# Performance work log

Measured on AMD Instinct MI355X. Metric: run time of the kernel, lower is better.

Reference implementation:

```python
import jax, jax.numpy as jnp
import numpy as np

N_NODES = 100000
N_EDGES = 3200000
N_GRAPHS = 64
HEADS = 8
NEG_SLOPE = 0.2


def gat_conv(x, W, a_src, a_dst, b, src, dst, heads, out_ch):
    """PyG GATConv (concat=True, add_self_loops=True, negative_slope=0.2, eval mode).
    x: [N, F_in]; W: [F_in, heads*out_ch]; a_src/a_dst: [heads, out_ch]; b: [heads*out_ch].
    src/dst already include self loops. Softmax over edges sharing a dst node.
    """
    n = x.shape[0]
    h = (x @ W).reshape(n, heads, out_ch)            # [N, H, C]
    alpha_src = jnp.einsum('nhc,hc->nh', h, a_src)   # [N, H]
    alpha_dst = jnp.einsum('nhc,hc->nh', h, a_dst)   # [N, H]
    e = jax.nn.leaky_relu(alpha_src[src] + alpha_dst[dst], NEG_SLOPE)  # [E, H]
    m = jax.ops.segment_max(e, dst, num_segments=n)
    e = jnp.exp(e - m[dst])
    denom = jax.ops.segment_sum(e, dst, num_segments=n)
    alpha = e / (denom[dst] + 1e-16)                 # [E, H]
    msg = alpha[:, :, None] * h[src]                 # [E, H, C]
    out = jax.ops.segment_sum(msg, dst, num_segments=n)  # [N, H, C]
    return out.reshape(n, heads * out_ch) + b


def setup_inputs() -> dict:
    key = jax.random.key(0)
    ks = jax.random.split(key, 24)
    x = jax.random.normal(ks[0], (N_NODES, 128), dtype=jnp.float32)
    edge_index = jax.random.randint(ks[1], (2, N_EDGES), 0, N_NODES, dtype=jnp.int32)
    batch = jnp.sort(jax.random.randint(ks[2], (N_NODES,), 0, N_GRAPHS, dtype=jnp.int32))

    def glorot(k, shape):
        fan_in, fan_out = shape[0], shape[-1]
        lim = np.sqrt(6.0 / (fan_in + fan_out)).astype(np.float32)
        return jax.random.uniform(k, shape, jnp.float32, -lim, lim)

    params = {
        'W1': glorot(ks[3], (128, 64)),
        'a_src1': glorot(ks[4], (HEADS, 8)),
        'a_dst1': glorot(ks[5], (HEADS, 8)),
        'b1': jnp.zeros((64,), jnp.float32),
        'W2': glorot(ks[6], (64, 128)),
        'a_src2': glorot(ks[7], (HEADS, 16)),
        'a_dst2': glorot(ks[8], (HEADS, 16)),
        'b2': jnp.zeros((128,), jnp.float32),
        'fc1_w': glorot(ks[9], (128, 256)),  'fc1_b': jnp.zeros((256,), jnp.float32),
        'fc2_w': glorot(ks[10], (256, 512)), 'fc2_b': jnp.zeros((512,), jnp.float32),
        'fc3_w': glorot(ks[11], (512, 512)), 'fc3_b': jnp.zeros((512,), jnp.float32),
        'fc4_w': glorot(ks[12], (512, 100)), 'fc4_b': jnp.zeros((100,), jnp.float32),
    }
    return {'x': x, 'edge_index': edge_index, 'batch': batch, **params}


def reference(x, edge_index, batch,
              W1, a_src1, a_dst1, b1,
              W2, a_src2, a_dst2, b2,
              fc1_w, fc1_b, fc2_w, fc2_b, fc3_w, fc3_b, fc4_w, fc4_b):
    n = x.shape[0]
    loop = jnp.arange(n, dtype=edge_index.dtype)
    src = jnp.concatenate([edge_index[0], loop])
    dst = jnp.concatenate([edge_index[1], loop])

    h = gat_conv(x, W1, a_src1, a_dst1, b1, src, dst, HEADS, 8)
    h = jax.nn.relu(h)
    h = gat_conv(h, W2, a_src2, a_dst2, b2, src, dst, HEADS, 16)
    h = jax.nn.relu(h)

    # global_mean_pool over batch ids
    sums = jax.ops.segment_sum(h, batch, num_segments=N_GRAPHS)        # [G, 128]
    counts = jax.ops.segment_sum(jnp.ones((n,), h.dtype), batch, num_segments=N_GRAPHS)
    g = sums / jnp.maximum(counts, 1.0)[:, None]

    g = jax.nn.relu(g @ fc1_w + fc1_b)
    g = jax.nn.relu(g @ fc2_w + fc2_b)
    g = jax.nn.relu(g @ fc3_w + fc3_b)
    g = g @ fc4_w + fc4_b
    return g.reshape(-1, 10, 10)
```

## Files before the change

### kernel.cpp

```cpp
#include <hip/hip_runtime.h>
#include <hip/hip_bf16.h>

#define NN 100000
#define NE 3200000
#define ET (NE + NN)
#define NG 64
#define BINBITS 10
#define NBINS 98
#define EPB 16
#define LOG2E 1.44269504088896f

__device__ __forceinline__ unsigned bfr(float x) {
  unsigned u = __float_as_uint(x);
  return (u + 0x7FFFu + ((u >> 16) & 1u)) >> 16;
}

__device__ __forceinline__ unsigned fkey(float x) {
  unsigned b = __float_as_uint(x);
  return (b & 0x80000000u) ? ~b : (b | 0x80000000u);
}

__device__ __forceinline__ float gmax_decode(unsigned k) {
  return __uint_as_float((k & 0x80000000u) ? (k & 0x7FFFFFFFu) : ~k);
}

__global__ void init_counts_k(int* counts) {
  int i = blockIdx.x * 256 + threadIdx.x;
  if (i < NN) counts[i] = 1;
}

__global__ void count_k(const int* __restrict__ dst, int* __restrict__ counts) {
  int i = blockIdx.x * 256 + threadIdx.x;
  if (i < NE) atomicAdd(&counts[dst[i]], 1);
}

__global__ __launch_bounds__(1024) void scan1_k(const int* __restrict__ cnt, int* __restrict__ csum) {
  __shared__ int lds[1024];
  int i = blockIdx.x * 1024 + threadIdx.x;
  lds[threadIdx.x] = (i < NN) ? cnt[i] : 0;
  __syncthreads();
  for (int off = 512; off > 0; off >>= 1) {
    if (threadIdx.x < off) lds[threadIdx.x] += lds[threadIdx.x + off];
    __syncthreads();
  }
  if (threadIdx.x == 0) csum[blockIdx.x] = lds[0];
}

__global__ __launch_bounds__(128) void scan2_k(int* csum, int nch) {
  __shared__ int lds[128];
  int v = (threadIdx.x < nch) ? csum[threadIdx.x] : 0;
  lds[threadIdx.x] = v;
  __syncthreads();
  for (int off = 1; off < 128; off <<= 1) {
    int t = (threadIdx.x >= off) ? lds[threadIdx.x - off] : 0;
    __syncthreads();
    lds[threadIdx.x] += t;
    __syncthreads();
  }
  if (threadIdx.x < nch) csum[threadIdx.x] = lds[threadIdx.x] - v;
}

__global__ __launch_bounds__(1024) void scan3_k(const int* __restrict__ cnt, const int* __restrict__ csum,
                                                int* __restrict__ indptr, int* __restrict__ cursor) {
  __shared__ int lds[1024];
  int i = blockIdx.x * 1024 + threadIdx.x;
  int v = (i < NN) ? cnt[i] : 0;
  lds[threadIdx.x] = v;
  __syncthreads();
  for (int off = 1; off < 1024; off <<= 1) {
    int t = (threadIdx.x >= off) ? lds[threadIdx.x - off] : 0;
    __syncthreads();
    lds[threadIdx.x] += t;
    __syncthreads();
  }
  int excl = csum[blockIdx.x] + lds[threadIdx.x] - v;
  if (i < NN) { indptr[i] = excl; cursor[i] = excl; }
  else if (i == NN) indptr[NN] = ET;
}

__global__ void bininit_k(const int* __restrict__ indptr, int* __restrict__ binbase, int* __restrict__ bincur) {
  int b = threadIdx.x;
  if (b <= NBINS) {
    int node = b << BINBITS; if (node > NN) node = NN;
    int v = indptr[node];
    binbase[b] = v;
    if (b < NBINS) bincur[b] = v;
  }
}

__global__ __launch_bounds__(256) void binA_k(const int* __restrict__ ei, int* __restrict__ bincur,
                                              unsigned* __restrict__ binbuf) {
  __shared__ int lhist[NBINS], lbase[NBINS];
  int t = threadIdx.x;
  for (int i = t; i < NBINS; i += 256) lhist[i] = 0;
  __syncthreads();
  long base = (long)blockIdx.x * (256 * EPB);
  unsigned pk[EPB]; int bn[EPB];
  #pragma unroll
  for (int j = 0; j < EPB; j++) {
    long i = base + j * 256 + t;
    if (i < ET) {
      int s, d;
      if (i < NE) { s = ei[i]; d = ei[NE + i]; }
      else { s = (int)(i - NE); d = s; }
      int b = d >> BINBITS;
      bn[j] = b;
      pk[j] = ((unsigned)s << BINBITS) | (unsigned)(d & 1023);
      atomicAdd(&lhist[b], 1);
    } else bn[j] = -1;
  }
  __syncthreads();
  for (int i = t; i < NBINS; i += 256) {
    int c = lhist[i];
    lbase[i] = c ? atomicAdd(&bincur[i], c) : 0;
    lhist[i] = 0;
  }
  __syncthreads();
  #pragma unroll
  for (int j = 0; j < EPB; j++) {
    if (bn[j] >= 0) {
      int off = atomicAdd(&lhist[bn[j]], 1);
      binbuf[lbase[bn[j]] + off] = pk[j];
    }
  }
}

#define SEGS 8
__global__ __launch_bounds__(256) void binB_k(const unsigned* __restrict__ binbuf, const int* __restrict__ binbase,
                                              int* __restrict__ cursor, int* __restrict__ srcs) {
  int r = blockIdx.x & 7;
  int m = blockIdx.x >> 3;
  int q = m / SEGS, seg = m % SEGS;
  int bin = q * 8 + r;
  if (bin >= NBINS) return;
  int b0 = binbase[bin], b1 = binbase[bin + 1];
  int n = b1 - b0;
  int per = (n + SEGS - 1) / SEGS;
  int e0 = b0 + seg * per;
  int e1 = min(e0 + per, b1);
  int dbase = bin << BINBITS;
  for (int i = e0 + threadIdx.x; i < e1; i += 256) {
    unsigned p = binbuf[i];
    int d = dbase | (int)(p & 1023u);
    int s = (int)(p >> BINBITS);
    int slot = atomicAdd(&cursor[d], 1);
    srcs[slot] = s;
  }
}

__global__ __launch_bounds__(256) void gemm1_k(const float* __restrict__ x, const float* __restrict__ W,
                                               const float* __restrict__ a_s, const float* __restrict__ a_d,
                                               unsigned* __restrict__ h1bf, float* __restrict__ asrc,
                                               float* __restrict__ adst, unsigned* __restrict__ gmaxg) {
  __shared__ float ldsW[128 * 64];
  __shared__ float ldsX[64 * 132];
  __shared__ unsigned gm8[8];
  int t = threadIdx.x;
  int n0 = blockIdx.x * 64;
  if (t < 8) gm8[t] = 0;
  {
    const float4* W4 = (const float4*)W;
    float4* lw = (float4*)ldsW;
    #pragma unroll
    for (int r = 0; r < 8; r++) lw[r * 256 + t] = W4[r * 256 + t];
  }
  #pragma unroll
  for (int r = 0; r < 8; r++) {
    int flat = r * 256 + t;
    int node = flat >> 5, kq = flat & 31;
    int gn = n0 + node;
    float4 v = make_float4(0.f, 0.f, 0.f, 0.f);
    if (gn < NN) v = ((const float4*)x)[(size_t)gn * 32 + kq];
    *(float4*)&ldsX[node * 132 + kq * 4] = v;
  }
  __syncthreads();
  int cg = t & 15, ng = t >> 4;
  float acc[4][4] = {};
  #pragma unroll 4
  for (int k = 0; k < 128; k += 2) {
    float2 xv0 = *(const float2*)&ldsX[(ng * 4 + 0) * 132 + k];
    float2 xv1 = *(const float2*)&ldsX[(ng * 4 + 1) * 132 + k];
    float2 xv2 = *(const float2*)&ldsX[(ng * 4 + 2) * 132 + k];
    float2 xv3 = *(const float2*)&ldsX[(ng * 4 + 3) * 132 + k];
    float4 w0 = *(const float4*)&ldsW[k * 64 + cg * 4];
    float4 w1 = *(const float4*)&ldsW[(k + 1) * 64 + cg * 4];
    acc[0][0] += xv0.x * w0.x + xv0.y * w1.x;
    acc[0][1] += xv0.x * w0.y + xv0.y * w1.y;
    acc[0][2] += xv0.x * w0.z + xv0.y * w1.z;
    acc[0][3] += xv0.x * w0.w + xv0.y * w1.w;
    acc[1][0] += xv1.x * w0.x + xv1.y * w1.x;
    acc[1][1] += xv1.x * w0.y + xv1.y * w1.y;
    acc[1][2] += xv1.x * w0.z + xv1.y * w1.z;
    acc[1][3] += xv1.x * w0.w + xv1.y * w1.w;
    acc[2][0] += xv2.x * w0.x + xv2.y * w1.x;
    acc[2][1] += xv2.x * w0.y + xv2.y * w1.y;
    acc[2][2] += xv2.x * w0.z + xv2.y * w1.z;
    acc[2][3] += xv2.x * w0.w + xv2.y * w1.w;
    acc[3][0] += xv3.x * w0.x + xv3.y * w1.x;
    acc[3][1] += xv3.x * w0.y + xv3.y * w1.y;
    acc[3][2] += xv3.x * w0.z + xv3.y * w1.z;
    acc[3][3] += xv3.x * w0.w + xv3.y * w1.w;
  }
  int head = cg >> 1, sub = (cg & 1) * 4;
  float as0 = a_s[head * 8 + sub], as1 = a_s[head * 8 + sub + 1];
  float as2 = a_s[head * 8 + sub + 2], as3 = a_s[head * 8 + sub + 3];
  float ad0 = a_d[head * 8 + sub], ad1 = a_d[head * 8 + sub + 1];
  float ad2 = a_d[head * 8 + sub + 2], ad3 = a_d[head * 8 + sub + 3];
  #pragma unroll
  for (int i = 0; i < 4; i++) {
    float vs = acc[i][0] * as0 + acc[i][1] * as1 + acc[i][2] * as2 + acc[i][3] * as3;
    float vd = acc[i][0] * ad0 + acc[i][1] * ad1 + acc[i][2] * ad2 + acc[i][3] * ad3;
    vs += __shfl_xor(vs, 1, 64);
    vd += __shfl_xor(vd, 1, 64);
    vs *= LOG2E; vd *= LOG2E;
    int gn = n0 + ng * 4 + i;
    if (gn < NN) {
      unsigned p0 = bfr(acc[i][0]) | (bfr(acc[i][1]) << 16);
      unsigned p1 = bfr(acc[i][2]) | (bfr(acc[i][3]) << 16);
      ((uint2*)(h1bf + (size_t)gn * 32))[cg] = make_uint2(p0, p1);
      if ((cg & 1) == 0) {
        asrc[gn * 8 + head] = vs;
        adst[gn * 8 + head] = vd;
        atomicMax(&gm8[head], fkey(vs));
      }
    }
  }
  __syncthreads();
  if (t < 8) atomicMax(&gmaxg[t], gm8[t]);
}

__global__ __launch_bounds__(256) void agg1_k(const unsigned* __restrict__ h1bf, const float* __restrict__ asrc,
                                              const float* __restrict__ adst_, const int* __restrict__ indptr,
                                              const int* __restrict__ srcs, const float* __restrict__ b,
                                              const unsigned* __restrict__ gmax, float* __restrict__ z1) {
  int wave = threadIdx.x >> 6, lane = threadIdx.x & 63;
  int node = blockIdx.x * 4 + wave;
  int s0 = indptr[node], s1 = indptr[node + 1];
  int grp = lane >> 4, q = lane & 15;
  int head = q >> 1;
  float ad = adst_[node * 8 + head];
  float ub = gmax_decode(gmax[head]) + ad; ub = fmaxf(ub, 0.2f * ub);
  const uint2* hp = (const uint2*)h1bf;
  float d = 0.f, a0 = 0.f, a1 = 0.f, a2 = 0.f, a3 = 0.f;
  for (int base = s0; base < s1; base += 64) {
    int i = base + lane;
    int sv = (i < s1) ? srcs[i] : 0;
    int n = s1 - base; if (n > 64) n = 64;
    for (int j = 0; j < n; j += 4) {
      int jj = j + grp;
      int s = __shfl(sv, jj, 64);
      float e = asrc[s * 8 + head] + ad;
      e = fmaxf(e, 0.2f * e);
      float w = __builtin_amdgcn_exp2f(e - ub);
      if (jj >= n) w = 0.f;
      uint2 u = hp[(size_t)s * 16 + q];
      d += w;
      a0 += w * __uint_as_float(u.x << 16);
      a1 += w * __uint_as_float(u.x & 0xFFFF0000u);
      a2 += w * __uint_as_float(u.y << 16);
      a3 += w * __uint_as_float(u.y & 0xFFFF0000u);
    }
  }
  d  += __shfl_xor(d, 16, 64);  d  += __shfl_xor(d, 32, 64);
  a0 += __shfl_xor(a0, 16, 64); a0 += __shfl_xor(a0, 32, 64);
  a1 += __shfl_xor(a1, 16, 64); a1 += __shfl_xor(a1, 32, 64);
  a2 += __shfl_xor(a2, 16, 64); a2 += __shfl_xor(a2, 32, 64);
  a3 += __shfl_xor(a3, 16, 64); a3 += __shfl_xor(a3, 32, 64);
  if (grp == 0) {
    float inv = 1.f / (d + 1e-16f);
    float o0 = a0 * inv + b[4 * q];
    float o1 = a1 * inv + b[4 * q + 1];
    float o2 = a2 * inv + b[4 * q + 2];
    float o3 = a3 * inv + b[4 * q + 3];
    float4 ov;
    ov.x = o0 > 0.f ? o0 : 0.f;
    ov.y = o1 > 0.f ? o1 : 0.f;
    ov.z = o2 > 0.f ? o2 : 0.f;
    ov.w = o3 > 0.f ? o3 : 0.f;
    ((float4*)z1)[node * 16 + q] = ov;
  }
}

__global__ __launch_bounds__(256) void gemm2_k(const float* __restrict__ z1, const float* __restrict__ W,
                                               const float* __restrict__ a_s, const float* __restrict__ a_d,
                                               uint2* __restrict__ h2bf, float* __restrict__ asrc,
                                               float* __restrict__ adst, unsigned* __restrict__ gmaxg) {
  __shared__ float ldsW[64 * 128];
  __shared__ float ldsZ[64 * 68];
  __shared__ unsigned gm8[8];
  int t = threadIdx.x;
  int n0 = blockIdx.x * 64;
  if (t < 8) gm8[t] = 0;
  {
    const float4* W4 = (const float4*)W;
    float4* lw = (float4*)ldsW;
    #pragma unroll
    for (int r = 0; r < 8; r++) lw[r * 256 + t] = W4[r * 256 + t];
  }
  #pragma unroll
  for (int r = 0; r < 4; r++) {
    int flat = r * 256 + t;
    int node = flat >> 4, kq = flat & 15;
    int gn = n0 + node;
    float4 v = make_float4(0.f, 0.f, 0.f, 0.f);
    if (gn < NN) v = ((const float4*)z1)[(size_t)gn * 16 + kq];
    *(float4*)&ldsZ[node * 68 + kq * 4] = v;
  }
  __syncthreads();
  int cg = t & 15, ng = t >> 4;
  int c0 = cg * 8;
  float acc[4][8] = {};
  #pragma unroll 2
  for (int k = 0; k < 64; k += 2) {
    float2 xv[4];
    #pragma unroll
    for (int i = 0; i < 4; i++) xv[i] = *(const float2*)&ldsZ[(ng * 4 + i) * 68 + k];
    float4 wa0 = *(const float4*)&ldsW[k * 128 + c0];
    float4 wa1 = *(const float4*)&ldsW[k * 128 + c0 + 4];
    float4 wb0 = *(const float4*)&ldsW[(k + 1) * 128 + c0];
    float4 wb1 = *(const float4*)&ldsW[(k + 1) * 128 + c0 + 4];
    #pragma unroll
    for (int i = 0; i < 4; i++) {
      acc[i][0] += xv[i].x * wa0.x + xv[i].y * wb0.x;
      acc[i][1] += xv[i].x * wa0.y + xv[i].y * wb0.y;
      acc[i][2] += xv[i].x * wa0.z + xv[i].y * wb0.z;
      acc[i][3] += xv[i].x * wa0.w + xv[i].y * wb0.w;
      acc[i][4] += xv[i].x * wa1.x + xv[i].y * wb1.x;
      acc[i][5] += xv[i].x * wa1.y + xv[i].y * wb1.y;
      acc[i][6] += xv[i].x * wa1.z + xv[i].y * wb1.z;
      acc[i][7] += xv[i].x * wa1.w + xv[i].y * wb1.w;
    }
  }
  int head = cg >> 1, sub = (cg & 1) * 8;
  float asv[8], adv[8];
  #pragma unroll
  for (int j = 0; j < 8; j++) {
    asv[j] = a_s[head * 16 + sub + j];
    adv[j] = a_d[head * 16 + sub + j];
  }
  #pragma unroll
  for (int i = 0; i < 4; i++) {
    float vs = 0.f, vd = 0.f;
    #pragma unroll
    for (int j = 0; j < 8; j++) { vs += acc[i][j] * asv[j]; vd += acc[i][j] * adv[j]; }
    vs += __shfl_xor(vs, 1, 64);
    vd += __shfl_xor(vd, 1, 64);
    vs *= LOG2E; vd *= LOG2E;
    int gn = n0 + ng * 4 + i;
    if (gn < NN) {
      unsigned p0 = bfr(acc[i][0]) | (bfr(acc[i][1]) << 16);
      unsigned p1 = bfr(acc[i][2]) | (bfr(acc[i][3]) << 16);
      unsigned p2 = bfr(acc[i][4]) | (bfr(acc[i][5]) << 16);
      unsigned p3 = bfr(acc[i][6]) | (bfr(acc[i][7]) << 16);
      ((uint4*)h2bf)[(size_t)gn * 16 + cg] = make_uint4(p0, p1, p2, p3);
      if ((cg & 1) == 0) {
        asrc[gn * 8 + head] = vs;
        adst[gn * 8 + head] = vd;
        atomicMax(&gm8[head], fkey(vs));
      }
    }
  }
  __syncthreads();
  if (t < 8) atomicMax(&gmaxg[t], gm8[t]);
}

__global__ __launch_bounds__(256) void agg2_k(const uint2* __restrict__ h2bf, const float* __restrict__ asrc,
                                              const float* __restrict__ adst_, const int* __restrict__ indptr,
                                              const int* __restrict__ srcs, const float* __restrict__ b,
                                              const unsigned* __restrict__ gmax, float* __restrict__ z2) {
  int wave = threadIdx.x >> 6, lane = threadIdx.x & 63;
  int node = blockIdx.x * 4 + wave;
  int s0 = indptr[node], s1 = indptr[node + 1];
  int grp = lane >> 4, q = lane & 15;
  int head = q >> 1;
  float ad = adst_[node * 8 + head];
  float ub = gmax_decode(gmax[head]) + ad; ub = fmaxf(ub, 0.2f * ub);
  const uint4* hp = (const uint4*)h2bf;
  float d = 0.f;
  float a0 = 0.f, a1 = 0.f, a2 = 0.f, a3 = 0.f, a4 = 0.f, a5 = 0.f, a6 = 0.f, a7 = 0.f;
  for (int base = s0; base < s1; base += 64) {
    int i = base + lane;
    int sv = (i < s1) ? srcs[i] : 0;
    int n = s1 - base; if (n > 64) n = 64;
    for (int j = 0; j < n; j += 4) {
      int jj = j + grp;
      int s = __shfl(sv, jj, 64);
      float e = asrc[s * 8 + head] + ad;
      e = fmaxf(e, 0.2f * e);
      float w = __builtin_amdgcn_exp2f(e - ub);
      if (jj >= n) w = 0.f;
      uint4 u = hp[(size_t)s * 16 + q];
      d += w;
      a0 += w * __uint_as_float(u.x << 16);
      a1 += w * __uint_as_float(u.x & 0xFFFF0000u);
      a2 += w * __uint_as_float(u.y << 16);
      a3 += w * __uint_as_float(u.y & 0xFFFF0000u);
      a4 += w * __uint_as_float(u.z << 16);
      a5 += w * __uint_as_float(u.z & 0xFFFF0000u);
      a6 += w * __uint_as_float(u.w << 16);
      a7 += w * __uint_as_float(u.w & 0xFFFF0000u);
    }
  }
  d  += __shfl_xor(d, 16, 64);  d  += __shfl_xor(d, 32, 64);
  a0 += __shfl_xor(a0, 16, 64); a0 += __shfl_xor(a0, 32, 64);
  a1 += __shfl_xor(a1, 16, 64); a1 += __shfl_xor(a1, 32, 64);
  a2 += __shfl_xor(a2, 16, 64); a2 += __shfl_xor(a2, 32, 64);
  a3 += __shfl_xor(a3, 16, 64); a3 += __shfl_xor(a3, 32, 64);
  a4 += __shfl_xor(a4, 16, 64); a4 += __shfl_xor(a4, 32, 64);
  a5 += __shfl_xor(a5, 16, 64); a5 += __shfl_xor(a5, 32, 64);
  a6 += __shfl_xor(a6, 16, 64); a6 += __shfl_xor(a6, 32, 64);
  a7 += __shfl_xor(a7, 16, 64); a7 += __shfl_xor(a7, 32, 64);
  if (grp == 0) {
    float inv = 1.f / (d + 1e-16f);
    float o0 = a0 * inv + b[8 * q];
    float o1 = a1 * inv + b[8 * q + 1];
    float o2 = a2 * inv + b[8 * q + 2];
    float o3 = a3 * inv + b[8 * q + 3];
    float o4 = a4 * inv + b[8 * q + 4];
    float o5 = a5 * inv + b[8 * q + 5];
    float o6 = a6 * inv + b[8 * q + 6];
    float o7 = a7 * inv + b[8 * q + 7];
    float4 v0, v1;
    v0.x = o0 > 0.f ? o0 : 0.f;
    v0.y = o1 > 0.f ? o1 : 0.f;
    v0.z = o2 > 0.f ? o2 : 0.f;
    v0.w = o3 > 0.f ? o3 : 0.f;
    v1.x = o4 > 0.f ? o4 : 0.f;
    v1.y = o5 > 0.f ? o5 : 0.f;
    v1.z = o6 > 0.f ? o6 : 0.f;
    v1.w = o7 > 0.f ? o7 : 0.f;
    ((float4*)z2)[node * 32 + 2 * q] = v0;
    ((float4*)z2)[node * 32 + 2 * q + 1] = v1;
  }
}

#define POOL_NODES 512
__global__ __launch_bounds__(128) void pool_k(const float* __restrict__ h, const int* __restrict__ batch,
                                              float* __restrict__ sums, float* __restrict__ cnts) {
  int ch = threadIdx.x;
  int base = blockIdx.x * POOL_NODES;
  int end = min(base + POOL_NODES, NN);
  float acc = 0.f; int cnt = 0; int cur = batch[base];
  for (int i = base; i < end; i++) {
    int g = batch[i];
    if (g != cur) {
      atomicAdd(&sums[cur * 128 + ch], acc);
      if (ch == 0) atomicAdd(&cnts[cur], (float)cnt);
      acc = 0.f; cnt = 0; cur = g;
    }
    acc += h[(size_t)i * 128 + ch];
    cnt++;
  }
  atomicAdd(&sums[cur * 128 + ch], acc);
  if (ch == 0) atomicAdd(&cnts[cur], (float)cnt);
}

__global__ void pooldiv_k(const float* __restrict__ sums, const float* __restrict__ cnts, float* __restrict__ g) {
  int i = blockIdx.x * 256 + threadIdx.x;
  if (i < NG * 128) {
    float c = cnts[i >> 7];
    c = c < 1.f ? 1.f : c;
    g[i] = sums[i] / c;
  }
}

template <int K, int OUT, bool RELU>
__global__ __launch_bounds__(256) void mlpg_k(const float* __restrict__ in, const float* __restrict__ W,
                                              const float* __restrict__ bias, float* __restrict__ out) {
  __shared__ float At[64][68];
  __shared__ float Bt[64][68];
  int t = threadIdx.x;
  int c0 = blockIdx.x * 64;
  int tg = t >> 5;
  int to = t & 31;
  float acc[8][2] = {};
  for (int kc = 0; kc < K; kc += 64) {
    #pragma unroll
    for (int r = 0; r < 4; r++) {
      int flat = r * 256 + t;
      int g = flat >> 4, kq = flat & 15;
      float4 v = *(const float4*)&in[g * K + kc + kq * 4];
      *(float4*)&At[g][kq * 4] = v;
    }
    #pragma unroll
    for (int r = 0; r < 4; r++) {
      int flat = r * 256 + t;
      int k = flat >> 4, cq = flat & 15;
      int col = c0 + cq * 4;
      float4 v = make_float4(0.f, 0.f, 0.f, 0.f);
      if (col < OUT) v = *(const float4*)&W[(size_t)(kc + k) * OUT + col];
      *(float4*)&Bt[k][cq * 4] = v;
    }
    __syncthreads();
    for (int k = 0; k < 64; k++) {
      float bv0 = Bt[k][to * 2], bv1 = Bt[k][to * 2 + 1];
      #pragma unroll
      for (int i = 0; i < 8; i++) {
        float av = At[tg * 8 + i][k];
        acc[i][0] += av * bv0;
        acc[i][1] += av * bv1;
      }
    }
    __syncthreads();
  }
  int col = c0 + to * 2;
  if (col < OUT) {
    float b0 = bias[col], b1 = bias[col + 1];
    #pragma unroll
    for (int i = 0; i < 8; i++) {
      int g = tg * 8 + i;
      float o0 = acc[i][0] + b0, o1 = acc[i][1] + b1;
      if (RELU) { o0 = fmaxf(o0, 0.f); o1 = fmaxf(o1, 0.f); }
      out[g * OUT + col] = o0;
      out[g * OUT + col + 1] = o1;
    }
  }
}

extern "C" void kernel_launch(void* const* d_in, const int* in_sizes, int n_in,
                              void* d_out, int out_size, void* d_ws, size_t ws_size,
                              hipStream_t stream) {
  const float* x      = (const float*)d_in[0];
  const int*   ei     = (const int*)d_in[1];
  const int*   batch  = (const int*)d_in[2];
  const float* W1     = (const float*)d_in[3];
  const float* a_src1 = (const float*)d_in[4];
  const float* a_dst1 = (const float*)d_in[5];
  const float* b1     = (const float*)d_in[6];
  const float* W2     = (const float*)d_in[7];
  const float* a_src2 = (const float*)d_in[8];
  const float* a_dst2 = (const float*)d_in[9];
  const float* b2     = (const float*)d_in[10];
  const float* fc1_w  = (const float*)d_in[11];
  const float* fc1_b  = (const float*)d_in[12];
  const float* fc2_w  = (const float*)d_in[13];
  const float* fc2_b  = (const float*)d_in[14];
  const float* fc3_w  = (const float*)d_in[15];
  const float* fc3_b  = (const float*)d_in[16];
  const float* fc4_w  = (const float*)d_in[17];
  const float* fc4_b  = (const float*)d_in[18];
  float* outp = (float*)d_out;

  float* z2   = (float*)d_ws;
  uint2* h2bf = (uint2*)(z2 + (size_t)NN * 128);
  float* asrc = (float*)(h2bf + (size_t)NN * 32);
  float* adst = asrc + (size_t)NN * 8;
  int* srcs   = (int*)(adst + (size_t)NN * 8);
  int* indptr = srcs + ET;
  float* sums = (float*)(indptr + NN + 1);
  float* gcnt = sums + NG * 128;
  float* mlp0 = gcnt + NG;
  float* mlp1 = mlp0 + NG * 512;
  unsigned* gmax = (unsigned*)(mlp1 + NG * 512);
  int* binbase = (int*)(gmax + 8);
  int* bincur  = binbase + NBINS + 1;
  unsigned* binbuf = (unsigned*)z2;
  int* counts = (int*)z2 + ET;
  int* cursor = counts + NN;
  unsigned* h1bf = (unsigned*)z2;
  float* z1 = z2 + (size_t)NN * 32;

  const int NCH = (NN + 1023) / 1024;

  init_counts_k<<<(NN + 255) / 256, 256, 0, stream>>>(counts);
  count_k<<<(NE + 255) / 256, 256, 0, stream>>>(ei + NE, counts);
  scan1_k<<<NCH, 1024, 0, stream>>>(counts, srcs);
  scan2_k<<<1, 128, 0, stream>>>(srcs, NCH);
  scan3_k<<<NCH, 1024, 0, stream>>>(counts, srcs, indptr, cursor);
  bininit_k<<<1, 128, 0, stream>>>(indptr, binbase, bincur);
  binA_k<<<(ET + 256 * EPB - 1) / (256 * EPB), 256, 0, stream>>>(ei, bincur, binbuf);
  {
    int nq = (NBINS + 7) / 8;
    int grid = 8 * nq * SEGS;
    binB_k<<<grid, 256, 0, stream>>>(binbuf, binbase, cursor, srcs);
  }

  const int NGEMM = (NN + 63) / 64;

  hipMemsetAsync(gmax, 0, 8 * sizeof(unsigned), stream);
  gemm1_k<<<NGEMM, 256, 0, stream>>>(x, W1, a_src1, a_dst1, h1bf, asrc, adst, gmax);
  agg1_k<<<NN / 4, 256, 0, stream>>>(h1bf, asrc, adst, indptr, srcs, b1, gmax, z1);

  hipMemsetAsync(gmax, 0, 8 * sizeof(unsigned), stream);
  gemm2_k<<<NGEMM, 256, 0, stream>>>(z1, W2, a_src2, a_dst2, h2bf, asrc, adst, gmax);
  agg2_k<<<NN / 4, 256, 0, stream>>>(h2bf, asrc, adst, indptr, srcs, b2, gmax, z2);

  hipMemsetAsync(sums, 0, (NG * 128 + NG) * sizeof(float), stream);
  pool_k<<<(NN + POOL_NODES - 1) / POOL_NODES, 128, 0, stream>>>(z2, batch, sums, gcnt);
  pooldiv_k<<<(NG * 128 + 255) / 256, 256, 0, stream>>>(sums, gcnt, mlp0);

  mlpg_k<128, 256, true><<<4, 256, 0, stream>>>(mlp0, fc1_w, fc1_b, mlp1);
  mlpg_k<256, 512, true><<<8, 256, 0, stream>>>(mlp1, fc2_w, fc2_b, mlp0);
  mlpg_k<512, 512, true><<<8, 256, 0, stream>>>(mlp0, fc3_w, fc3_b, mlp1);
  mlpg_k<512, 100, false><<<2, 256, 0, stream>>>(mlp1, fc4_w, fc4_b, outp);

  (void)in_sizes; (void)n_in; (void)out_size; (void)ws_size;
}
```

Baseline: 847.6 us.

## Fuse pooling divide and MLP head into one kernel; read GEMM inputs directly

The mean-divide and four MLP layers are replaced by a single kernel with one block per graph, keeping activations in shared memory and removing five launches plus intermediate global buffers. Separately, gemm1 and gemm2 no longer stage node features in LDS; each thread reads its four rows straight from global memory via clamped pointers. This lowers LDS use, which may raise occupancy, but the per-thread float2 loads are strided across rows and uncoalesced. The fused MLP uses only 64 blocks and re-reads the weights once per graph.

Result: no change. 852.2 us (+0.5%).

```diff
diff --git a/kernel.cpp b/kernel.cpp
--- a/kernel.cpp
+++ b/kernel.cpp
@@ -153,7 +153,6 @@
                                                unsigned* __restrict__ h1bf, float* __restrict__ asrc,
                                                float* __restrict__ adst, unsigned* __restrict__ gmaxg) {
   __shared__ float ldsW[128 * 64];
-  __shared__ float ldsX[64 * 132];
   __shared__ unsigned gm8[8];
   int t = threadIdx.x;
   int n0 = blockIdx.x * 64;
@@ -164,24 +163,19 @@
     #pragma unroll
     for (int r = 0; r < 8; r++) lw[r * 256 + t] = W4[r * 256 + t];
   }
-  #pragma unroll
-  for (int r = 0; r < 8; r++) {
-    int flat = r * 256 + t;
-    int node = flat >> 5, kq = flat & 31;
-    int gn = n0 + node;
-    float4 v = make_float4(0.f, 0.f, 0.f, 0.f);
-    if (gn < NN) v = ((const float4*)x)[(size_t)gn * 32 + kq];
-    *(float4*)&ldsX[node * 132 + kq * 4] = v;
-  }
   __syncthreads();
   int cg = t & 15, ng = t >> 4;
+  const float* xr0 = x + (size_t)min(n0 + ng * 4 + 0, NN - 1) * 128;
+  const float* xr1 = x + (size_t)min(n0 + ng * 4 + 1, NN - 1) * 128;
+  const float* xr2 = x + (size_t)min(n0 + ng * 4 + 2, NN - 1) * 128;
+  const float* xr3 = x + (size_t)min(n0 + ng * 4 + 3, NN - 1) * 128;
   float acc[4][4] = {};
   #pragma unroll 4
   for (int k = 0; k < 128; k += 2) {
-    float2 xv0 = *(const float2*)&ldsX[(ng * 4 + 0) * 132 + k];
-    float2 xv1 = *(const float2*)&ldsX[(ng * 4 + 1) * 132 + k];
-    float2 xv2 = *(const float2*)&ldsX[(ng * 4 + 2) * 132 + k];
-    float2 xv3 = *(const float2*)&ldsX[(ng * 4 + 3) * 132 + k];
+    float2 xv0 = *(const float2*)&xr0[k];
+    float2 xv1 = *(const float2*)&xr1[k];
+    float2 xv2 = *(const float2*)&xr2[k];
+    float2 xv3 = *(const float2*)&xr3[k];
     float4 w0 = *(const float4*)&ldsW[k * 64 + cg * 4];
     float4 w1 = *(const float4*)&ldsW[(k + 1) * 64 + cg * 4];
     acc[0][0] += xv0.x * w0.x + xv0.y * w1.x;
@@ -286,7 +280,6 @@
                                                uint2* __restrict__ h2bf, float* __restrict__ asrc,
                                                float* __restrict__ adst, unsigned* __restrict__ gmaxg) {
   __shared__ float ldsW[64 * 128];
-  __shared__ float ldsZ[64 * 68];
   __shared__ unsigned gm8[8];
   int t = threadIdx.x;
   int n0 = blockIdx.x * 64;
@@ -297,24 +290,21 @@
     #pragma unroll
     for (int r = 0; r < 8; r++) lw[r * 256 + t] = W4[r * 256 + t];
   }
-  #pragma unroll
-  for (int r = 0; r < 4; r++) {
-    int flat = r * 256 + t;
-    int node = flat >> 4, kq = flat & 15;
-    int gn = n0 + node;
-    float4 v = make_float4(0.f, 0.f, 0.f, 0.f);
-    if (gn < NN) v = ((const float4*)z1)[(size_t)gn * 16 + kq];
-    *(float4*)&ldsZ[node * 68 + kq * 4] = v;
-  }
   __syncthreads();
   int cg = t & 15, ng = t >> 4;
   int c0 = cg * 8;
+  const float* zr0 = z1 + (size_t)min(n0 + ng * 4 + 0, NN - 1) * 64;
+  const float* zr1 = z1 + (size_t)min(n0 + ng * 4 + 1, NN - 1) * 64;
+  const float* zr2 = z1 + (size_t)min(n0 + ng * 4 + 2, NN - 1) * 64;
+  const float* zr3 = z1 + (size_t)min(n0 + ng * 4 + 3, NN - 1) * 64;
   float acc[4][8] = {};
   #pragma unroll 2
   for (int k = 0; k < 64; k += 2) {
     float2 xv[4];
-    #pragma unroll
-    for (int i = 0; i < 4; i++) xv[i] = *(const float2*)&ldsZ[(ng * 4 + i) * 68 + k];
+    xv[0] = *(const float2*)&zr0[k];
+    xv[1] = *(const float2*)&zr1[k];
+    xv[2] = *(const float2*)&zr2[k];
+    xv[3] = *(const float2*)&zr3[k];
     float4 wa0 = *(const float4*)&ldsW[k * 128 + c0];
     float4 wa1 = *(const float4*)&ldsW[k * 128 + c0 + 4];
     float4 wb0 = *(const float4*)&ldsW[(k + 1) * 128 + c0];
@@ -455,65 +445,53 @@
   if (ch == 0) atomicAdd(&cnts[cur], (float)cnt);
 }
 
-__global__ void pooldiv_k(const float* __restrict__ sums, const float* __restrict__ cnts, float* __restrict__ g) {
-  int i = blockIdx.x * 256 + threadIdx.x;
-  if (i < NG * 128) {
-    float c = cnts[i >> 7];
-    c = c < 1.f ? 1.f : c;
-    g[i] = sums[i] / c;
-  }
-}
-
-template <int K, int OUT, bool RELU>
-__global__ __launch_bounds__(256) void mlpg_k(const float* __restrict__ in, const float* __restrict__ W,
-                                              const float* __restrict__ bias, float* __restrict__ out) {
-  __shared__ float At[64][68];
-  __shared__ float Bt[64][68];
-  int t = threadIdx.x;
-  int c0 = blockIdx.x * 64;
-  int tg = t >> 5;
-  int to = t & 31;
-  float acc[8][2] = {};
-  for (int kc = 0; kc < K; kc += 64) {
-    #pragma unroll
-    for (int r = 0; r < 4; r++) {
-      int flat = r * 256 + t;
-      int g = flat >> 4, kq = flat & 15;
-      float4 v = *(const float4*)&in[g * K + kc + kq * 4];
-      *(float4*)&At[g][kq * 4] = v;
-    }
-    #pragma unroll
-    for (int r = 0; r < 4; r++) {
-      int flat = r * 256 + t;
-      int k = flat >> 4, cq = flat & 15;
-      int col = c0 + cq * 4;
-      float4 v = make_float4(0.f, 0.f, 0.f, 0.f);
-      if (col < OUT) v = *(const float4*)&W[(size_t)(kc + k) * OUT + col];
-      *(float4*)&Bt[k][cq * 4] = v;
-    }
-    __syncthreads();
-    for (int k = 0; k < 64; k++) {
-      float bv0 = Bt[k][to * 2], bv1 = Bt[k][to * 2 + 1];
-      #pragma unroll
-      for (int i = 0; i < 8; i++) {
-        float av = At[tg * 8 + i][k];
-        acc[i][0] += av * bv0;
-        acc[i][1] += av * bv1;
-      }
-    }
-    __syncthreads();
-  }
-  int col = c0 + to * 2;
-  if (col < OUT) {
-    float b0 = bias[col], b1 = bias[col + 1];
-    #pragma unroll
-    for (int i = 0; i < 8; i++) {
-      int g = tg * 8 + i;
-      float o0 = acc[i][0] + b0, o1 = acc[i][1] + b1;
-      if (RELU) { o0 = fmaxf(o0, 0.f); o1 = fmaxf(o1, 0.f); }
-      out[g * OUT + col] = o0;
-      out[g * OUT + col + 1] = o1;
-    }
+__global__ __launch_bounds__(256) void mlpfused_k(const float* __restrict__ sums, const float* __restrict__ cnts,
+                                                  const float* __restrict__ w1, const float* __restrict__ bb1,
+                                                  const float* __restrict__ w2, const float* __restrict__ bb2,
+                                                  const float* __restrict__ w3, const float* __restrict__ bb3,
+                                                  const float* __restrict__ w4, const float* __restrict__ bb4,
+                                                  float* __restrict__ out) {
+  __shared__ float bufA[512], bufB[512];
+  int g = blockIdx.x, t = threadIdx.x;
+  float inv = 1.f / fmaxf(cnts[g], 1.f);
+  if (t < 128) bufA[t] = sums[g * 128 + t] * inv;
+  __syncthreads();
+  {
+    float acc = bb1[t];
+    #pragma unroll 4
+    for (int k = 0; k < 128; k++) acc += bufA[k] * w1[k * 256 + t];
+    bufB[t] = fmaxf(acc, 0.f);
+  }
+  __syncthreads();
+  {
+    float a0 = bb2[t], a1 = bb2[t + 256];
+    #pragma unroll 4
+    for (int k = 0; k < 256; k++) {
+      float av = bufB[k];
+      a0 += av * w2[k * 512 + t];
+      a1 += av * w2[k * 512 + t + 256];
+    }
+    bufA[t] = fmaxf(a0, 0.f);
+    bufA[t + 256] = fmaxf(a1, 0.f);
+  }
+  __syncthreads();
+  {
+    float a0 = bb3[t], a1 = bb3[t + 256];
+    #pragma unroll 4
+    for (int k = 0; k < 512; k++) {
+      float av = bufA[k];
+      a0 += av * w3[k * 512 + t];
+      a1 += av * w3[k * 512 + t + 256];
+    }
+    bufB[t] = fmaxf(a0, 0.f);
+    bufB[t + 256] = fmaxf(a1, 0.f);
+  }
+  __syncthreads();
+  if (t < 100) {
+    float acc = bb4[t];
+    #pragma unroll 4
+    for (int k = 0; k < 512; k++) acc += bufB[k] * w4[k * 100 + t];
+    out[g * 100 + t] = acc;
   }
 }
 
@@ -549,9 +527,7 @@
   int* indptr = srcs + ET;
   float* sums = (float*)(indptr + NN + 1);
   float* gcnt = sums + NG * 128;
-  float* mlp0 = gcnt + NG;
-  float* mlp1 = mlp0 + NG * 512;
-  unsigned* gmax = (unsigned*)(mlp1 + NG * 512);
+  unsigned* gmax = (unsigned*)(gcnt + NG);
   int* binbase = (int*)(gmax + 8);
   int* bincur  = binbase + NBINS + 1;
   unsigned* binbuf = (unsigned*)z2;
@@ -587,12 +563,8 @@
 
   hipMemsetAsync(sums, 0, (NG * 128 + NG) * sizeof(float), stream);
   pool_k<<<(NN + POOL_NODES - 1) / POOL_NODES, 128, 0, stream>>>(z2, batch, sums, gcnt);
-  pooldiv_k<<<(NG * 128 + 255) / 256, 256, 0, stream>>>(sums, gcnt, mlp0);
-
-  mlpg_k<128, 256, true><<<4, 256, 0, stream>>>(mlp0, fc1_w, fc1_b, mlp1);
-  mlpg_k<256, 512, true><<<8, 256, 0, stream>>>(mlp1, fc2_w, fc2_b, mlp0);
-  mlpg_k<512, 512, true><<<8, 256, 0, stream>>>(mlp0, fc3_w, fc3_b, mlp1);
-  mlpg_k<512, 100, false><<<2, 256, 0, stream>>>(mlp1, fc4_w, fc4_b, outp);
+  mlpfused_k<<<NG, 256, 0, stream>>>(sums, gcnt, fc1_w, fc1_b, fc2_w, fc2_b,
+                                     fc3_w, fc3_b, fc4_w, fc4_b, outp);
 
   (void)in_sizes; (void)n_in; (void)out_size; (void)ws_size;
 }
```
